# Optimization experiments

Hardware: AMD Instinct MI355X
Metric: run time of the kernel (lower is better)

## Reference

```python
import jax, jax.numpy as jnp
import numpy as np

LAMBDA_SOFTMAX = 9.0
LAMBDA_LSE = 6.0
MARGIN = 0.2
EPS = 1e-8


def setup_inputs() -> dict:
    key = jax.random.key(0)
    k1, k2, k3 = jax.random.split(key, 3)
    Ni, R, W, d = 128, 36, 50, 1024
    im = jax.random.normal(k1, (Ni, R, d), dtype=jnp.float32)
    s = jax.random.normal(k2, (Ni, W, d), dtype=jnp.float32)
    s_l = jax.random.randint(k3, (Ni,), 5, W + 1, dtype=jnp.int32)
    return {"im": im, "s": s, "s_l": s_l}


def _scan_t2i_scores(im, s, s_l):
    # im: (Ni, R, d) images; s: (Nc, W, d) captions; s_l: (Nc,) caption lengths
    Nc, W, _ = s.shape
    word_mask = jnp.arange(W)[None, :] < s_l[:, None]          # (Nc, W)
    # attn[c,i,r,w] = <im[i,r], s[c,w]>  (bmm(context, query^T) per caption)
    attn = jnp.einsum('ird,cwd->cirw', im, s)                  # (Nc, Ni, R, W)
    # clipped_l2norm: LeakyReLU(0.1) then l2-normalize over word dim
    attn = jax.nn.leaky_relu(attn, 0.1)
    attn = attn * word_mask[:, None, None, :]                  # zero padded words
    norm = jnp.sqrt(jnp.sum(attn * attn, axis=3, keepdims=True)) + EPS
    attn = attn / norm
    # transpose to (Nc, Ni, W, R), smooth-softmax over regions
    attn_t = jax.nn.softmax(jnp.swapaxes(attn, 2, 3) * LAMBDA_SOFTMAX, axis=-1)
    # weighted image context per word: (Nc, Ni, W, d)
    wei = jnp.einsum('ird,ciwr->ciwd', im, attn_t)
    # cosine similarity along d between cap word and weighted context
    w12 = jnp.einsum('cwd,ciwd->ciw', s, wei)                  # (Nc, Ni, W)
    w1 = jnp.linalg.norm(s, axis=-1)                           # (Nc, W)
    w2 = jnp.linalg.norm(wei, axis=-1)                         # (Nc, Ni, W)
    row_sim = w12 / jnp.clip(w1[:, None, :] * w2, EPS, None)
    # LogSumExp aggregation over valid words only
    e = jnp.where(word_mask[:, None, :], jnp.exp(row_sim * LAMBDA_LSE), 0.0)
    sims = jnp.log(jnp.sum(e, axis=2)) / LAMBDA_LSE            # (Nc, Ni)
    return sims.T                                              # scores[i, c]


def reference(im, s, s_l) -> jnp.ndarray:
    scores = _scan_t2i_scores(im, s, s_l)                      # (Ni, Nc), Ni == Nc
    diag = jnp.diag(scores)[:, None]
    cost_s = jnp.clip(MARGIN + scores - diag, 0.0, None)       # caption retrieval
    cost_im = jnp.clip(MARGIN + scores - diag.T, 0.0, None)    # image retrieval
    eye = jnp.eye(scores.shape[0], dtype=bool)
    cost_s = jnp.where(eye, 0.0, cost_s)
    cost_im = jnp.where(eye, 0.0, cost_im)
    # max_violation=True: hardest negative per row/column
    return jnp.max(cost_s, axis=1).sum() + jnp.max(cost_im, axis=0).sum()
```

## Files before the change

kernel.cpp:

```cpp
#include <hip/hip_runtime.h>
#include <hip/hip_bf16.h>
#include <cstdint>

using u16 = unsigned short;
using u32 = unsigned int;
using bf16x8 = __attribute__((ext_vector_type(8))) short;
using f32x4  = __attribute__((ext_vector_type(4))) float;

#define NI 128
#define NC 128
#define RR 36
#define WW 50
#define DD 1024
#define LDC 6400
#define ATS 37
#define IMN ((size_t)NI * RR * DD)
#define SN  ((size_t)NC * WW * DD)

#define GLL16(g, l) __builtin_amdgcn_global_load_lds(                        \
    (const __attribute__((address_space(1))) void*)(g),                      \
    (__attribute__((address_space(3))) void*)(l), 16, 0, 0)

typedef const __attribute__((address_space(4))) float cfloat;

__device__ __forceinline__ float2 bf16pair(u32 u) {
  float2 f;
  f.x = __uint_as_float(u << 16);
  f.y = __uint_as_float(u & 0xffff0000u);
  return f;
}

__device__ __forceinline__ u32 bf16_rne(u32 x) {
  return (x + 0x7FFFu + ((x >> 16) & 1u)) >> 16;
}

__global__ __launch_bounds__(256) void convert_in(const void* __restrict__ im_in,
                                                  const void* __restrict__ s_in,
                                                  u16* __restrict__ imB,
                                                  u16* __restrict__ sB,
                                                  int* __restrict__ flag) {
  __shared__ int cnt;
  if (threadIdx.x == 0) cnt = 0;
  __syncthreads();
  const u16* imu = (const u16*)im_in;
  int local = 0;
#pragma unroll
  for (int v = 0; v < 16; ++v) {
    u16 u = imu[threadIdx.x * 16 + v];
    if (((u >> 7) & 0xFF) >= 0xC0) local++;
  }
  if (local) atomicAdd(&cnt, local);
  __syncthreads();
  const int f = (cnt > 4) ? 1 : 0;
  if (blockIdx.x == 0 && threadIdx.x == 0) *flag = f;
  if (!f) return;

  const size_t TOT8 = (IMN + SN) / 8;
  const size_t stride = (size_t)gridDim.x * blockDim.x;
  for (size_t g = (size_t)blockIdx.x * blockDim.x + threadIdx.x; g < TOT8; g += stride) {
    size_t base = g * 8;
    const u32* sp;
    u16* dst;
    if (base < IMN) { sp = (const u32*)im_in + base; dst = imB + base; }
    else            { sp = (const u32*)s_in + (base - IMN); dst = sB + (base - IMN); }
    u16 o[8];
#pragma unroll
    for (int e = 0; e < 8; ++e) o[e] = (u16)bf16_rne(sp[e]);
    *(uint4*)dst = *(const uint4*)o;
  }
}

__global__ __launch_bounds__(256) void gram_w1(const u16* __restrict__ im_orig,
                                               const u16* __restrict__ im_conv,
                                               const u16* __restrict__ s_orig,
                                               const u16* __restrict__ s_conv,
                                               const int* __restrict__ flag,
                                               float* __restrict__ G,
                                               float* __restrict__ w1) {
  const u16* im = *flag ? im_conv : im_orig;
  const u16* s  = *flag ? s_conv : s_orig;
  __shared__ u16 ims[48 * 520];
  const int b = blockIdx.x;
  const int t = threadIdx.x;
  const int lane = t & 63, wv = t >> 6;
  const int lm = lane & 15, q = lane >> 4;
  f32x4 acc[3][3] = {};

  for (int p = 0; p < 2; ++p) {
    const int kk = p * 512;
#pragma unroll
    for (int v = 0; v < 9; ++v) {
      int u = t + v * 256;
      int row = u >> 6;
      int kloc = (u & 63) * 8;
      uint4 val = *(const uint4*)(im + (size_t)b * (RR * DD) + (size_t)row * DD + kk + kloc);
      *(uint4*)&ims[row * 520 + kloc] = val;
    }
    if (p == 0) {
#pragma unroll
      for (int v = 0; v < 4; ++v) {
        int u = t + v * 256;
        if (u < 780) {
          uint4 z; z.x = 0; z.y = 0; z.z = 0; z.w = 0;
          *(uint4*)&ims[36 * 520 + u * 8] = z;
        }
      }
    }
    __syncthreads();
#pragma unroll
    for (int kq = 0; kq < 4; ++kq) {
      const int ks = wv * 4 + kq;
      bf16x8 af[3];
#pragma unroll
      for (int mi = 0; mi < 3; ++mi)
        af[mi] = *(const bf16x8*)&ims[(mi * 16 + lm) * 520 + ks * 32 + q * 8];
#pragma unroll
      for (int mi = 0; mi < 3; ++mi)
#pragma unroll
        for (int ni = 0; ni < 3; ++ni)
          acc[mi][ni] = __builtin_amdgcn_mfma_f32_16x16x32_bf16(af[mi], af[ni], acc[mi][ni], 0, 0, 0);
    }
    __syncthreads();
  }
  float* red = (float*)ims;
  if (wv > 0) {
#pragma unroll
    for (int mi = 0; mi < 3; ++mi)
#pragma unroll
      for (int ni = 0; ni < 3; ++ni)
#pragma unroll
        for (int v = 0; v < 4; ++v) {
          int row = mi * 16 + q * 4 + v;
          int col = ni * 16 + lm;
          red[(wv - 1) * 2304 + row * 48 + col] = acc[mi][ni][v];
        }
  }
  __syncthreads();
  if (wv == 0) {
#pragma unroll
    for (int mi = 0; mi < 3; ++mi)
#pragma unroll
      for (int ni = 0; ni < 3; ++ni)
#pragma unroll
        for (int v = 0; v < 4; ++v) {
          int row = mi * 16 + q * 4 + v;
          int col = ni * 16 + lm;
          float r0 = acc[mi][ni][v] + red[row * 48 + col] +
                     red[2304 + row * 48 + col] + red[4608 + row * 48 + col];
          if (row < RR && col < RR)
            G[(size_t)b * (RR * RR) + row * RR + col] = r0;
        }
  }
  const u16* sc = s + (size_t)b * WW * DD;
  for (int w = wv; w < WW; w += 4) {
    const u16* sp = sc + (size_t)w * DD + lane * 16;
    uint4 A0 = *(const uint4*)sp;
    uint4 A1 = *(const uint4*)(sp + 8);
    float sum = 0.f;
    u32 uu[8] = {A0.x, A0.y, A0.z, A0.w, A1.x, A1.y, A1.z, A1.w};
#pragma unroll
    for (int e = 0; e < 8; ++e) {
      float2 f = bf16pair(uu[e]);
      sum += f.x * f.x + f.y * f.y;
    }
#pragma unroll
    for (int off = 32; off > 0; off >>= 1) sum += __shfl_down(sum, off);
    if (lane == 0) w1[b * WW + w] = sqrtf(sum);
  }
}

__global__ __launch_bounds__(256) void gemm_raw(const u16* __restrict__ A_orig,
                                                const u16* __restrict__ A_conv,
                                                const u16* __restrict__ B_orig,
                                                const u16* __restrict__ B_conv,
                                                const int* __restrict__ flag,
                                                u16* __restrict__ C) {
  const u16* A = *flag ? A_conv : A_orig;
  const u16* B = *flag ? B_conv : B_orig;
  __shared__ u16 As[128 * 64];
  __shared__ u16 Bs[128 * 64];
  const int t = threadIdx.x;
  const int col0 = blockIdx.x * 128;
  const int row0 = blockIdx.y * 128;
  const int lane = t & 63, wv = t >> 6;
  const int wm = wv >> 1, wn = wv & 1;
  const int lm = lane & 15, q = lane >> 4;
  f32x4 acc[4][4] = {};

  const u16* ap[4];
  const u16* bp[4];
#pragma unroll
  for (int v = 0; v < 4; ++v) {
    int u = t + v * 256;
    int row = u >> 3;
    int c = (u & 7) ^ (row & 7);
    ap[v] = A + (size_t)(row0 + row) * DD + c * 8;
    bp[v] = B + (size_t)(col0 + row) * DD + c * 8;
  }

  for (int k0 = 0; k0 < DD; k0 += 64) {
#pragma unroll
    for (int v = 0; v < 4; ++v) GLL16(ap[v] + k0, &As[(t + v * 256) * 8]);
#pragma unroll
    for (int v = 0; v < 4; ++v) GLL16(bp[v] + k0, &Bs[(t + v * 256) * 8]);
    __syncthreads();
#pragma unroll
    for (int ks = 0; ks < 2; ++ks) {
      bf16x8 af[4], bf[4];
      const int pch = (ks * 4 + q) ^ (lm & 7);
#pragma unroll
      for (int mi = 0; mi < 4; ++mi)
        af[mi] = *(const bf16x8*)&As[(wm * 64 + mi * 16 + lm) * 64 + pch * 8];
#pragma unroll
      for (int ni = 0; ni < 4; ++ni)
        bf[ni] = *(const bf16x8*)&Bs[(wn * 64 + ni * 16 + lm) * 64 + pch * 8];
#pragma unroll
      for (int mi = 0; mi < 4; ++mi)
#pragma unroll
        for (int ni = 0; ni < 4; ++ni)
          acc[mi][ni] = __builtin_amdgcn_mfma_f32_16x16x32_bf16(af[mi], bf[ni], acc[mi][ni], 0, 0, 0);
    }
    __syncthreads();
  }
#pragma unroll
  for (int mi = 0; mi < 4; ++mi)
#pragma unroll
    for (int ni = 0; ni < 4; ++ni)
#pragma unroll
      for (int v = 0; v < 4; ++v) {
        int rr = row0 + wm * 64 + mi * 16 + q * 4 + v;
        int cc = col0 + wn * 64 + ni * 16 + lm;
        C[(size_t)rr * LDC + cc] = (u16)bf16_rne(__float_as_uint(acc[mi][ni][v]));
      }
}

__global__ __launch_bounds__(256, 2) void postproc(const u16* __restrict__ raw,
                                                   const float* __restrict__ G,
                                                   const float* __restrict__ w1,
                                                   const int* __restrict__ s_l,
                                                   float* __restrict__ scores) {
  const int i = blockIdx.y;
  const int wv = threadIdx.x >> 6;
  const int c = blockIdx.x * 4 + wv;
  const int lane = threadIdx.x & 63;
  __shared__ float aT[4][WW * ATS];
  __shared__ float nrm9_s[4][RR];
  const int L = s_l[c];

  if (lane < RR) {
    const u16* rp = raw + (size_t)(i * RR + lane) * LDC + c * WW;
    float sum = 0.f;
#pragma unroll
    for (int j = 0; j < 25; ++j) {
      float2 v = bf16pair(((const u32*)rp)[j]);
      float x0 = v.x > 0.f ? v.x : 0.1f * v.x;
      float x1 = v.y > 0.f ? v.y : 0.1f * v.y;
      if (2 * j     >= L) x0 = 0.f;
      if (2 * j + 1 >= L) x1 = 0.f;
      aT[wv][(2 * j) * ATS + lane]     = x0;
      aT[wv][(2 * j + 1) * ATS + lane] = x1;
      sum += x0 * x0 + x1 * x1;
    }
    nrm9_s[wv][lane] = 9.0f / (sqrtf(sum) + 1e-8f);
  }
  __syncthreads();

  const int wIdx = lane < WW ? lane : WW - 1;
  const float* row = &aT[wv][wIdx * ATS];
  cfloat* Gp = (cfloat*)(G + (size_t)i * (RR * RR));

  float x[RR];
  float m = -1e30f;
#pragma unroll
  for (int r = 0; r < RR; ++r) {
    x[r] = row[r];
    m = fmaxf(m, x[r] * nrm9_s[wv][r]);
  }
  float e[RR];
  float sum = 0.f, w12r = 0.f;
#pragma unroll
  for (int r = 0; r < RR; ++r) {
    float er = __expf(x[r] * nrm9_s[wv][r] - m);
    e[r] = er;
    sum += er;
    w12r += er * (x[r] > 0.f ? x[r] : 10.0f * x[r]);
  }
  float qq2 = 0.f;
#pragma unroll
  for (int r = 0; r < RR; ++r) {
    float h = 0.5f * Gp[r * RR + r] * e[r];
#pragma unroll
    for (int j = r + 1; j < RR; ++j)
      h += Gp[r * RR + j] * e[j];
    qq2 += e[r] * h;
  }
  float qq = 2.0f * qq2;
  float w1v = w1[c * WW + wIdx];
  float denom = fmaxf(w1v * sqrtf(fmaxf(qq, 0.f)), 1e-8f * sum);
  float rs = w12r / denom;
  float ew = (lane < L) ? __expf(6.0f * rs) : 0.f;
#pragma unroll
  for (int off = 32; off > 0; off >>= 1) ew += __shfl_down(ew, off);
  if (lane == 0) scores[i * NC + c] = logf(ew) * (1.0f / 6.0f);
}

__global__ __launch_bounds__(128) void loss_k(const float* __restrict__ scores,
                                              u32* __restrict__ out) {
  __shared__ float diag[NI];
  __shared__ float red[NI];
  const int t = threadIdx.x;
  diag[t] = scores[t * NC + t];
  __syncthreads();
  const float di = diag[t];
  float rowmax = 0.f, colmax = 0.f;
  for (int k = 0; k < NC; ++k) {
    if (k != t) {
      float sr = scores[t * NC + k];
      rowmax = fmaxf(rowmax, fmaxf(0.2f + sr - di, 0.f));
      float sc = scores[k * NC + t];
      colmax = fmaxf(colmax, fmaxf(0.2f + sc - di, 0.f));
    }
  }
  red[t] = rowmax + colmax;
  __syncthreads();
  for (int st = 64; st > 0; st >>= 1) {
    if (t < st) red[t] += red[t + st];
    __syncthreads();
  }
  if (t == 0) {
    u32 b = bf16_rne(__float_as_uint(red[0]));
    out[0] = b | (b << 16);
  }
}

extern "C" void kernel_launch(void* const* d_in, const int* in_sizes, int n_in,
                              void* d_out, int out_size, void* d_ws, size_t ws_size,
                              hipStream_t stream) {
  const void* im_in = d_in[0];
  const void* s_in  = d_in[1];
  const int*  sl    = (const int*)d_in[2];

  char* ws = (char*)d_ws;
  u16*   imB    = (u16*)ws;
  u16*   sB     = (u16*)(ws + 9437184);
  u16*   raw    = (u16*)(ws + 22544384);
  float* G      = (float*)(ws + 22544384 + 58982400);
  float* w1     = G + 128 * RR * RR;
  float* scores = w1 + NC * WW;
  int*   flag   = (int*)(scores + NI * NC);

  convert_in<<<dim3(2048), dim3(256), 0, stream>>>(im_in, s_in, imB, sB, flag);
  gram_w1<<<dim3(128), dim3(256), 0, stream>>>((const u16*)im_in, imB,
                                               (const u16*)s_in, sB, flag, G, w1);
  gemm_raw<<<dim3(50, 36), dim3(256), 0, stream>>>((const u16*)im_in, imB,
                                                   (const u16*)s_in, sB, flag, raw);
  postproc<<<dim3(32, 128), dim3(256), 0, stream>>>(raw, G, w1, sl, scores);
  loss_k<<<dim3(1), dim3(128), 0, stream>>>(scores, (u32*)d_out);
}
```

Measured before the change: 277.3 us.

## Fuse input conversion into GEMM and Gram kernels, fold loss into postproc

Drops the separate fp32-to-bf16 conversion pass: GEMM and Gram blocks now read fp32 inputs directly and pack them to bf16 while staging into LDS. The Gram/w1 work moves into the same launch as the GEMM as extra blocks. The loss kernel is folded into postproc through a last-block atomic counter. This removes a full extra read/write of the inputs and two launches. In exchange the fp32 path loses the async global-to-LDS loads and does synchronous converting loads inside the GEMM loop.

```diff
diff --git a/kernel.cpp b/kernel.cpp
--- a/kernel.cpp
+++ b/kernel.cpp
@@ -14,8 +14,8 @@
 #define DD 1024
 #define LDC 6400
 #define ATS 37
-#define IMN ((size_t)NI * RR * DD)
-#define SN  ((size_t)NC * WW * DD)
+#define GEMM_BLOCKS 1800
+#define POST_BLOCKS 4096
 
 #define GLL16(g, l) __builtin_amdgcn_global_load_lds(                        \
     (const __attribute__((address_space(1))) void*)(g),                      \
@@ -34,217 +34,232 @@
   return (x + 0x7FFFu + ((x >> 16) & 1u)) >> 16;
 }
 
-__global__ __launch_bounds__(256) void convert_in(const void* __restrict__ im_in,
+__device__ __forceinline__ uint4 pack8_bf16(float4 a, float4 b) {
+  u16 o[8] = {(u16)bf16_rne(__float_as_uint(a.x)), (u16)bf16_rne(__float_as_uint(a.y)),
+              (u16)bf16_rne(__float_as_uint(a.z)), (u16)bf16_rne(__float_as_uint(a.w)),
+              (u16)bf16_rne(__float_as_uint(b.x)), (u16)bf16_rne(__float_as_uint(b.y)),
+              (u16)bf16_rne(__float_as_uint(b.z)), (u16)bf16_rne(__float_as_uint(b.w))};
+  return *(const uint4*)o;
+}
+
+__global__ __launch_bounds__(256) void fused_main(const void* __restrict__ im_in,
                                                   const void* __restrict__ s_in,
-                                                  u16* __restrict__ imB,
-                                                  u16* __restrict__ sB,
-                                                  int* __restrict__ flag) {
+                                                  u16* __restrict__ raw,
+                                                  float* __restrict__ G,
+                                                  float* __restrict__ w1,
+                                                  int* __restrict__ counter) {
+  __shared__ __align__(16) char smem[32768];
   __shared__ int cnt;
-  if (threadIdx.x == 0) cnt = 0;
-  __syncthreads();
-  const u16* imu = (const u16*)im_in;
-  int local = 0;
-#pragma unroll
-  for (int v = 0; v < 16; ++v) {
-    u16 u = imu[threadIdx.x * 16 + v];
-    if (((u >> 7) & 0xFF) >= 0xC0) local++;
-  }
-  if (local) atomicAdd(&cnt, local);
-  __syncthreads();
-  const int f = (cnt > 4) ? 1 : 0;
-  if (blockIdx.x == 0 && threadIdx.x == 0) *flag = f;
-  if (!f) return;
-
-  const size_t TOT8 = (IMN + SN) / 8;
-  const size_t stride = (size_t)gridDim.x * blockDim.x;
-  for (size_t g = (size_t)blockIdx.x * blockDim.x + threadIdx.x; g < TOT8; g += stride) {
-    size_t base = g * 8;
-    const u32* sp;
-    u16* dst;
-    if (base < IMN) { sp = (const u32*)im_in + base; dst = imB + base; }
-    else            { sp = (const u32*)s_in + (base - IMN); dst = sB + (base - IMN); }
-    u16 o[8];
-#pragma unroll
-    for (int e = 0; e < 8; ++e) o[e] = (u16)bf16_rne(sp[e]);
-    *(uint4*)dst = *(const uint4*)o;
-  }
-}
-
-__global__ __launch_bounds__(256) void gram_w1(const u16* __restrict__ im_orig,
-                                               const u16* __restrict__ im_conv,
-                                               const u16* __restrict__ s_orig,
-                                               const u16* __restrict__ s_conv,
-                                               const int* __restrict__ flag,
-                                               float* __restrict__ G,
-                                               float* __restrict__ w1) {
-  const u16* im = *flag ? im_conv : im_orig;
-  const u16* s  = *flag ? s_conv : s_orig;
-  __shared__ u16 ims[48 * 520];
-  const int b = blockIdx.x;
   const int t = threadIdx.x;
+  const int id = blockIdx.x;
+  if (t == 0) { cnt = 0; if (id == 0) *counter = 0; }
+  __syncthreads();
+  {
+    uint4 sv = *(const uint4*)((const u16*)im_in + t * 8);
+    u32 ss[4] = {sv.x, sv.y, sv.z, sv.w};
+    int local = 0;
+#pragma unroll
+    for (int e = 0; e < 4; ++e) {
+      if (((ss[e] >> 7)  & 0xFF) >= 0xC0) local++;
+      if (((ss[e] >> 23) & 0xFF) >= 0xC0) local++;
+    }
+    if (local) atomicAdd(&cnt, local);
+  }
+  __syncthreads();
+  const bool f32in = cnt > 4;
+
   const int lane = t & 63, wv = t >> 6;
   const int lm = lane & 15, q = lane >> 4;
-  f32x4 acc[3][3] = {};
-
-  for (int p = 0; p < 2; ++p) {
-    const int kk = p * 512;
-#pragma unroll
-    for (int v = 0; v < 9; ++v) {
+
+  if (id < GEMM_BLOCKS) {
+    u16* As = (u16*)smem;
+    u16* Bs = (u16*)(smem + 16384);
+    const int col0 = (id % 50) * 128;
+    const int row0 = (id / 50) * 128;
+    const int wm = wv >> 1, wn = wv & 1;
+    f32x4 acc[4][4] = {};
+    int rowv[4], chv[4];
+#pragma unroll
+    for (int v = 0; v < 4; ++v) {
       int u = t + v * 256;
-      int row = u >> 6;
-      int kloc = (u & 63) * 8;
-      uint4 val = *(const uint4*)(im + (size_t)b * (RR * DD) + (size_t)row * DD + kk + kloc);
-      *(uint4*)&ims[row * 520 + kloc] = val;
-    }
-    if (p == 0) {
-#pragma unroll
-      for (int v = 0; v < 4; ++v) {
+      rowv[v] = u >> 3;
+      chv[v] = (u & 7) ^ (rowv[v] & 7);
+    }
+
+    for (int k0 = 0; k0 < DD; k0 += 64) {
+      if (!f32in) {
+        const u16* A = (const u16*)im_in;
+        const u16* B = (const u16*)s_in;
+#pragma unroll
+        for (int v = 0; v < 4; ++v)
+          GLL16(A + (size_t)(row0 + rowv[v]) * DD + chv[v] * 8 + k0,
+                &As[(t + v * 256) * 8]);
+#pragma unroll
+        for (int v = 0; v < 4; ++v)
+          GLL16(B + (size_t)(col0 + rowv[v]) * DD + chv[v] * 8 + k0,
+                &Bs[(t + v * 256) * 8]);
+      } else {
+        const float* A = (const float*)im_in;
+        const float* B = (const float*)s_in;
+#pragma unroll
+        for (int v = 0; v < 4; ++v) {
+          const float* pa = A + (size_t)(row0 + rowv[v]) * DD + chv[v] * 8 + k0;
+          *(uint4*)&As[(t + v * 256) * 8] =
+              pack8_bf16(*(const float4*)pa, *(const float4*)(pa + 4));
+          const float* pb = B + (size_t)(col0 + rowv[v]) * DD + chv[v] * 8 + k0;
+          *(uint4*)&Bs[(t + v * 256) * 8] =
+              pack8_bf16(*(const float4*)pb, *(const float4*)(pb + 4));
+        }
+      }
+      __syncthreads();
+#pragma unroll
+      for (int ks = 0; ks < 2; ++ks) {
+        bf16x8 af[4], bf[4];
+        const int pch = (ks * 4 + q) ^ (lm & 7);
+#pragma unroll
+        for (int mi = 0; mi < 4; ++mi)
+          af[mi] = *(const bf16x8*)&As[(wm * 64 + mi * 16 + lm) * 64 + pch * 8];
+#pragma unroll
+        for (int ni = 0; ni < 4; ++ni)
+          bf[ni] = *(const bf16x8*)&Bs[(wn * 64 + ni * 16 + lm) * 64 + pch * 8];
+#pragma unroll
+        for (int mi = 0; mi < 4; ++mi)
+#pragma unroll
+          for (int ni = 0; ni < 4; ++ni)
+            acc[mi][ni] = __builtin_amdgcn_mfma_f32_16x16x32_bf16(af[mi], bf[ni], acc[mi][ni], 0, 0, 0);
+      }
+      __syncthreads();
+    }
+#pragma unroll
+    for (int mi = 0; mi < 4; ++mi)
+#pragma unroll
+      for (int ni = 0; ni < 4; ++ni)
+#pragma unroll
+        for (int v = 0; v < 4; ++v) {
+          int rr = row0 + wm * 64 + mi * 16 + q * 4 + v;
+          int cc = col0 + wn * 64 + ni * 16 + lm;
+          raw[(size_t)rr * LDC + cc] = (u16)bf16_rne(__float_as_uint(acc[mi][ni][v]));
+        }
+  } else {
+    const int b = id - GEMM_BLOCKS;
+    u16* ims = (u16*)smem;
+    f32x4 acc[3][3] = {};
+
+    for (int p = 0; p < 4; ++p) {
+      const int kk = p * 256;
+#pragma unroll
+      for (int v = 0; v < 5; ++v) {
         int u = t + v * 256;
-        if (u < 780) {
-          uint4 z; z.x = 0; z.y = 0; z.z = 0; z.w = 0;
-          *(uint4*)&ims[36 * 520 + u * 8] = z;
-        }
-      }
+        if (u < 1152) {
+          int row = u >> 5;
+          int kloc = (u & 31) * 8;
+          uint4 val;
+          if (!f32in) {
+            val = *(const uint4*)((const u16*)im_in + (size_t)(b * RR + row) * DD + kk + kloc);
+          } else {
+            const float* p2 = (const float*)im_in + (size_t)(b * RR + row) * DD + kk + kloc;
+            val = pack8_bf16(*(const float4*)p2, *(const float4*)(p2 + 4));
+          }
+          *(uint4*)&ims[row * 264 + kloc] = val;
+        }
+      }
+      if (p == 0) {
+#pragma unroll
+        for (int v = 0; v < 2; ++v) {
+          int u = t + v * 256;
+          if (u < 396) {
+            uint4 z; z.x = 0; z.y = 0; z.z = 0; z.w = 0;
+            *(uint4*)&ims[36 * 264 + u * 8] = z;
+          }
+        }
+      }
+      __syncthreads();
+#pragma unroll
+      for (int kq = 0; kq < 2; ++kq) {
+        const int ks = wv * 2 + kq;
+        bf16x8 af[3];
+#pragma unroll
+        for (int mi = 0; mi < 3; ++mi)
+          af[mi] = *(const bf16x8*)&ims[(mi * 16 + lm) * 264 + ks * 32 + q * 8];
+#pragma unroll
+        for (int mi = 0; mi < 3; ++mi)
+#pragma unroll
+          for (int ni = 0; ni < 3; ++ni)
+            acc[mi][ni] = __builtin_amdgcn_mfma_f32_16x16x32_bf16(af[mi], af[ni], acc[mi][ni], 0, 0, 0);
+      }
+      __syncthreads();
+    }
+    float* red = (float*)smem;
+    if (wv > 0) {
+#pragma unroll
+      for (int mi = 0; mi < 3; ++mi)
+#pragma unroll
+        for (int ni = 0; ni < 3; ++ni)
+#pragma unroll
+          for (int v = 0; v < 4; ++v) {
+            int row = mi * 16 + q * 4 + v;
+            int col = ni * 16 + lm;
+            red[(wv - 1) * 2304 + row * 48 + col] = acc[mi][ni][v];
+          }
     }
     __syncthreads();
-#pragma unroll
-    for (int kq = 0; kq < 4; ++kq) {
-      const int ks = wv * 4 + kq;
-      bf16x8 af[3];
+    if (wv == 0) {
 #pragma unroll
       for (int mi = 0; mi < 3; ++mi)
-        af[mi] = *(const bf16x8*)&ims[(mi * 16 + lm) * 520 + ks * 32 + q * 8];
-#pragma unroll
-      for (int mi = 0; mi < 3; ++mi)
 #pragma unroll
         for (int ni = 0; ni < 3; ++ni)
-          acc[mi][ni] = __builtin_amdgcn_mfma_f32_16x16x32_bf16(af[mi], af[ni], acc[mi][ni], 0, 0, 0);
-    }
-    __syncthreads();
-  }
-  float* red = (float*)ims;
-  if (wv > 0) {
-#pragma unroll
-    for (int mi = 0; mi < 3; ++mi)
-#pragma unroll
-      for (int ni = 0; ni < 3; ++ni)
-#pragma unroll
-        for (int v = 0; v < 4; ++v) {
-          int row = mi * 16 + q * 4 + v;
-          int col = ni * 16 + lm;
-          red[(wv - 1) * 2304 + row * 48 + col] = acc[mi][ni][v];
-        }
-  }
-  __syncthreads();
-  if (wv == 0) {
-#pragma unroll
-    for (int mi = 0; mi < 3; ++mi)
-#pragma unroll
-      for (int ni = 0; ni < 3; ++ni)
-#pragma unroll
-        for (int v = 0; v < 4; ++v) {
-          int row = mi * 16 + q * 4 + v;
-          int col = ni * 16 + lm;
-          float r0 = acc[mi][ni][v] + red[row * 48 + col] +
-                     red[2304 + row * 48 + col] + red[4608 + row * 48 + col];
-          if (row < RR && col < RR)
-            G[(size_t)b * (RR * RR) + row * RR + col] = r0;
-        }
-  }
-  const u16* sc = s + (size_t)b * WW * DD;
-  for (int w = wv; w < WW; w += 4) {
-    const u16* sp = sc + (size_t)w * DD + lane * 16;
-    uint4 A0 = *(const uint4*)sp;
-    uint4 A1 = *(const uint4*)(sp + 8);
-    float sum = 0.f;
-    u32 uu[8] = {A0.x, A0.y, A0.z, A0.w, A1.x, A1.y, A1.z, A1.w};
-#pragma unroll
-    for (int e = 0; e < 8; ++e) {
-      float2 f = bf16pair(uu[e]);
-      sum += f.x * f.x + f.y * f.y;
-    }
-#pragma unroll
-    for (int off = 32; off > 0; off >>= 1) sum += __shfl_down(sum, off);
-    if (lane == 0) w1[b * WW + w] = sqrtf(sum);
-  }
-}
-
-__global__ __launch_bounds__(256) void gemm_raw(const u16* __restrict__ A_orig,
-                                                const u16* __restrict__ A_conv,
-                                                const u16* __restrict__ B_orig,
-                                                const u16* __restrict__ B_conv,
-                                                const int* __restrict__ flag,
-                                                u16* __restrict__ C) {
-  const u16* A = *flag ? A_conv : A_orig;
-  const u16* B = *flag ? B_conv : B_orig;
-  __shared__ u16 As[128 * 64];
-  __shared__ u16 Bs[128 * 64];
-  const int t = threadIdx.x;
-  const int col0 = blockIdx.x * 128;
-  const int row0 = blockIdx.y * 128;
-  const int lane = t & 63, wv = t >> 6;
-  const int wm = wv >> 1, wn = wv & 1;
-  const int lm = lane & 15, q = lane >> 4;
-  f32x4 acc[4][4] = {};
-
-  const u16* ap[4];
-  const u16* bp[4];
-#pragma unroll
-  for (int v = 0; v < 4; ++v) {
-    int u = t + v * 256;
-    int row = u >> 3;
-    int c = (u & 7) ^ (row & 7);
-    ap[v] = A + (size_t)(row0 + row) * DD + c * 8;
-    bp[v] = B + (size_t)(col0 + row) * DD + c * 8;
-  }
-
-  for (int k0 = 0; k0 < DD; k0 += 64) {
-#pragma unroll
-    for (int v = 0; v < 4; ++v) GLL16(ap[v] + k0, &As[(t + v * 256) * 8]);
-#pragma unroll
-    for (int v = 0; v < 4; ++v) GLL16(bp[v] + k0, &Bs[(t + v * 256) * 8]);
-    __syncthreads();
-#pragma unroll
-    for (int ks = 0; ks < 2; ++ks) {
-      bf16x8 af[4], bf[4];
-      const int pch = (ks * 4 + q) ^ (lm & 7);
-#pragma unroll
-      for (int mi = 0; mi < 4; ++mi)
-        af[mi] = *(const bf16x8*)&As[(wm * 64 + mi * 16 + lm) * 64 + pch * 8];
-#pragma unroll
-      for (int ni = 0; ni < 4; ++ni)
-        bf[ni] = *(const bf16x8*)&Bs[(wn * 64 + ni * 16 + lm) * 64 + pch * 8];
-#pragma unroll
-      for (int mi = 0; mi < 4; ++mi)
-#pragma unroll
-        for (int ni = 0; ni < 4; ++ni)
-          acc[mi][ni] = __builtin_amdgcn_mfma_f32_16x16x32_bf16(af[mi], bf[ni], acc[mi][ni], 0, 0, 0);
-    }
-    __syncthreads();
-  }
-#pragma unroll
-  for (int mi = 0; mi < 4; ++mi)
-#pragma unroll
-    for (int ni = 0; ni < 4; ++ni)
-#pragma unroll
-      for (int v = 0; v < 4; ++v) {
-        int rr = row0 + wm * 64 + mi * 16 + q * 4 + v;
-        int cc = col0 + wn * 64 + ni * 16 + lm;
-        C[(size_t)rr * LDC + cc] = (u16)bf16_rne(__float_as_uint(acc[mi][ni][v]));
-      }
+#pragma unroll
+          for (int v = 0; v < 4; ++v) {
+            int row = mi * 16 + q * 4 + v;
+            int col = ni * 16 + lm;
+            float r0 = acc[mi][ni][v] + red[row * 48 + col] +
+                       red[2304 + row * 48 + col] + red[4608 + row * 48 + col];
+            if (row < RR && col < RR)
+              G[(size_t)b * (RR * RR) + row * RR + col] = r0;
+          }
+    }
+    for (int w = wv; w < WW; w += 4) {
+      float sum = 0.f;
+      if (!f32in) {
+        const u16* sp = (const u16*)s_in + ((size_t)b * WW + w) * DD + lane * 16;
+        uint4 A0 = *(const uint4*)sp;
+        uint4 A1 = *(const uint4*)(sp + 8);
+        u32 uu[8] = {A0.x, A0.y, A0.z, A0.w, A1.x, A1.y, A1.z, A1.w};
+#pragma unroll
+        for (int e = 0; e < 8; ++e) {
+          float2 f = bf16pair(uu[e]);
+          sum += f.x * f.x + f.y * f.y;
+        }
+      } else {
+        const float* sp = (const float*)s_in + ((size_t)b * WW + w) * DD + lane * 16;
+#pragma unroll
+        for (int e = 0; e < 4; ++e) {
+          float4 fv = *(const float4*)(sp + e * 4);
+          sum += fv.x * fv.x + fv.y * fv.y + fv.z * fv.z + fv.w * fv.w;
+        }
+      }
+#pragma unroll
+      for (int off = 32; off > 0; off >>= 1) sum += __shfl_down(sum, off);
+      if (lane == 0) w1[b * WW + w] = sqrtf(sum);
+    }
+  }
 }
 
 __global__ __launch_bounds__(256, 2) void postproc(const u16* __restrict__ raw,
                                                    const float* __restrict__ G,
                                                    const float* __restrict__ w1,
                                                    const int* __restrict__ s_l,
-                                                   float* __restrict__ scores) {
+                                                   float* __restrict__ scores,
+                                                   int* __restrict__ counter,
+                                                   u32* __restrict__ out) {
   const int i = blockIdx.y;
   const int wv = threadIdx.x >> 6;
   const int c = blockIdx.x * 4 + wv;
   const int lane = threadIdx.x & 63;
   __shared__ float aT[4][WW * ATS];
   __shared__ float nrm9_s[4][RR];
+  __shared__ float red2[NI];
+  __shared__ int lastBlk;
   const int L = s_l[c];
 
   if (lane < RR) {
@@ -302,34 +317,37 @@
 #pragma unroll
   for (int off = 32; off > 0; off >>= 1) ew += __shfl_down(ew, off);
   if (lane == 0) scores[i * NC + c] = logf(ew) * (1.0f / 6.0f);
-}
-
-__global__ __launch_bounds__(128) void loss_k(const float* __restrict__ scores,
-                                              u32* __restrict__ out) {
-  __shared__ float diag[NI];
-  __shared__ float red[NI];
-  const int t = threadIdx.x;
-  diag[t] = scores[t * NC + t];
-  __syncthreads();
-  const float di = diag[t];
-  float rowmax = 0.f, colmax = 0.f;
-  for (int k = 0; k < NC; ++k) {
-    if (k != t) {
-      float sr = scores[t * NC + k];
-      rowmax = fmaxf(rowmax, fmaxf(0.2f + sr - di, 0.f));
-      float sc = scores[k * NC + t];
-      colmax = fmaxf(colmax, fmaxf(0.2f + sc - di, 0.f));
-    }
-  }
-  red[t] = rowmax + colmax;
-  __syncthreads();
-  for (int st = 64; st > 0; st >>= 1) {
-    if (t < st) red[t] += red[t + st];
+
+  __threadfence();
+  __syncthreads();
+  if (threadIdx.x == 0)
+    lastBlk = (atomicAdd(counter, 1) == POST_BLOCKS - 1);
+  __syncthreads();
+  if (lastBlk) {
+    __threadfence();
+    const int t = threadIdx.x;
+    if (t < NI) {
+      float di = scores[t * NC + t];
+      float rowmax = 0.f, colmax = 0.f;
+      for (int k = 0; k < NC; ++k) {
+        if (k != t) {
+          float sr = scores[t * NC + k];
+          rowmax = fmaxf(rowmax, fmaxf(0.2f + sr - di, 0.f));
+          float sc = scores[k * NC + t];
+          colmax = fmaxf(colmax, fmaxf(0.2f + sc - di, 0.f));
+        }
+      }
+      red2[t] = rowmax + colmax;
+    }
     __syncthreads();
-  }
-  if (t == 0) {
-    u32 b = bf16_rne(__float_as_uint(red[0]));
-    out[0] = b | (b << 16);
+    for (int st = 64; st > 0; st >>= 1) {
+      if (t < st) red2[t] += red2[t + st];
+      __syncthreads();
+    }
+    if (t == 0) {
+      u32 b = bf16_rne(__float_as_uint(red2[0]));
+      out[0] = b | (b << 16);
+    }
   }
 }
 
@@ -341,19 +359,14 @@
   const int*  sl    = (const int*)d_in[2];
 
   char* ws = (char*)d_ws;
-  u16*   imB    = (u16*)ws;
-  u16*   sB     = (u16*)(ws + 9437184);
-  u16*   raw    = (u16*)(ws + 22544384);
-  float* G      = (float*)(ws + 22544384 + 58982400);
+  u16*   raw    = (u16*)ws;
+  float* G      = (float*)(ws + 58982400);
   float* w1     = G + 128 * RR * RR;
   float* scores = w1 + NC * WW;
-  int*   flag   = (int*)(scores + NI * NC);
-
-  convert_in<<<dim3(2048), dim3(256), 0, stream>>>(im_in, s_in, imB, sB, flag);
-  gram_w1<<<dim3(128), dim3(256), 0, stream>>>((const u16*)im_in, imB,
-                                               (const u16*)s_in, sB, flag, G, w1);
-  gemm_raw<<<dim3(50, 36), dim3(256), 0, stream>>>((const u16*)im_in, imB,
-                                                   (const u16*)s_in, sB, flag, raw);
-  postproc<<<dim3(32, 128), dim3(256), 0, stream>>>(raw, G, w1, sl, scores);
-  loss_k<<<dim3(1), dim3(128), 0, stream>>>(scores, (u32*)d_out);
-}
+  int*   counter = (int*)(scores + NI * NC);
+
+  fused_main<<<dim3(GEMM_BLOCKS + 128), dim3(256), 0, stream>>>(
+      im_in, s_in, raw, G, w1, counter);
+  postproc<<<dim3(32, 128), dim3(256), 0, stream>>>(
+      raw, G, w1, sl, scores, counter, (u32*)d_out);
+}
```

Result: slower. 634.3 us (+128.7%).
